# Kernel tuning notes

Hardware: AMD Instinct MI355X
Metric: run time of the kernel (lower is better)

Reference implementation:

```python
import jax, jax.numpy as jnp
import numpy as np

INPUT_SIZE = 1024
HIDDEN = 1024
NUM_LAYERS = 1
BATCH = 64
SEQ = 512


def setup_inputs() -> dict:
    key = jax.random.key(0)
    ks = jax.random.split(key, 5)
    stdv = 1.0 / np.sqrt(HIDDEN)
    u = lambda k, shape: jax.random.uniform(k, shape, jnp.float32, -stdv, stdv)
    x = jax.random.normal(ks[0], (BATCH, SEQ, INPUT_SIZE), dtype=jnp.float32)
    Wi = u(ks[1], (INPUT_SIZE, 4 * HIDDEN))
    Wh = u(ks[2], (HIDDEN, 4 * HIDDEN))
    bi = u(ks[3], (4 * HIDDEN,))
    bh = u(ks[4], (4 * HIDDEN,))
    return {"x": x, "Wi": Wi, "Wh": Wh, "bi": bi, "bh": bh}


def reference(x, Wi, Wh, bi, bh):
    B, T, _ = x.shape
    H = Wh.shape[0]
    L = NUM_LAYERS
    h0 = jnp.zeros((L, B, H), x.dtype)
    c0 = jnp.zeros((L, B, H), x.dtype)
    b = bi + bh  # fuse bias add

    def step(carry, xt):
        h, c = carry
        gates = xt @ Wi + h[-1] @ Wh + b  # [B, 4H]
        i_g, f_g, g_g, o_g = jnp.split(gates, 4, axis=1)
        i_g = jax.nn.sigmoid(i_g)
        f_g = jax.nn.sigmoid(f_g)
        g_g = jnp.tanh(g_g)
        o_g = jax.nn.sigmoid(o_g)
        c = f_g * c + i_g * g_g          # broadcasts [B,H] over [L,B,H]
        h = o_g * jnp.tanh(c)
        return (h, c), h

    (h, c), hs = jax.lax.scan(step, (h0, c0), jnp.swapaxes(x, 0, 1))
    # hs: [T, L, B, H] -> output [L, T, B, H] matching torch cat along dim=1
    output = jnp.swapaxes(hs, 0, 1)
    return output, h, c
```

## Files before the change

### kernel.cpp

```cpp
#include <hip/hip_runtime.h>
#include <math.h>

#define I_SZ 1024
#define H_SZ 1024
#define FH   4096
#define B_SZ 64
#define T_SZ 512

typedef _Float16 half8 __attribute__((ext_vector_type(8)));
typedef float    f32x4 __attribute__((ext_vector_type(4)));

#define MiB (1u << 20)
#define SLOT_HALFS 65536


__global__ __launch_bounds__(256) void k_cvt_wT(const float* __restrict__ W,
                                                _Float16* __restrict__ WT) {
  int tid = blockIdx.x * 256 + threadIdx.x;
  int n  = tid & (FH - 1);
  int k8 = tid >> 12;
  half8 h;
#pragma unroll
  for (int j = 0; j < 8; j++) h[j] = (_Float16)W[(size_t)(k8 * 8 + j) * FH + n];
  *(half8*)(WT + (size_t)n * 1024 + k8 * 8) = h;
}

__global__ __launch_bounds__(256) void k_gemm_pre(
    const float* __restrict__ x, const _Float16* __restrict__ WiT,
    const float* __restrict__ bi, const float* __restrict__ bh,
    _Float16* __restrict__ G) {
  __shared__ _Float16 As[128][40];
  __shared__ _Float16 Bs[128][40];
  const int tn = blockIdx.x, tm = blockIdx.y;
  const int tx = threadIdx.x;
  const int l = tx & 63, wv = tx >> 6;
  const int wm = wv & 1, wn = wv >> 1;
  const int r0 = tx >> 2, q0 = tx & 3;
  const int m0 = tm * 128 + r0, m1 = m0 + 64;
  const float* aR0 = x + (size_t)((m0 & 63) * T_SZ + (m0 >> 6)) * I_SZ + q0 * 8;
  const float* aR1 = x + (size_t)((m1 & 63) * T_SZ + (m1 >> 6)) * I_SZ + q0 * 8;
  const _Float16* bR0 = WiT + (size_t)(tn * 128 + r0) * 1024 + q0 * 8;
  const _Float16* bR1 = WiT + (size_t)(tn * 128 + 64 + r0) * 1024 + q0 * 8;

  f32x4 acc[4][4];
#pragma unroll
  for (int a = 0; a < 4; a++)
#pragma unroll
    for (int b = 0; b < 4; b++) acc[a][b] = {0.f, 0.f, 0.f, 0.f};

  for (int kt = 0; kt < 32; kt++) {
    __syncthreads();
    float4 va0 = *(const float4*)(aR0 + kt * 32);
    float4 va1 = *(const float4*)(aR0 + kt * 32 + 4);
    float4 vb0 = *(const float4*)(aR1 + kt * 32);
    float4 vb1 = *(const float4*)(aR1 + kt * 32 + 4);
    half8 ha, hb;
    ha[0] = (_Float16)va0.x; ha[1] = (_Float16)va0.y; ha[2] = (_Float16)va0.z; ha[3] = (_Float16)va0.w;
    ha[4] = (_Float16)va1.x; ha[5] = (_Float16)va1.y; ha[6] = (_Float16)va1.z; ha[7] = (_Float16)va1.w;
    hb[0] = (_Float16)vb0.x; hb[1] = (_Float16)vb0.y; hb[2] = (_Float16)vb0.z; hb[3] = (_Float16)vb0.w;
    hb[4] = (_Float16)vb1.x; hb[5] = (_Float16)vb1.y; hb[6] = (_Float16)vb1.z; hb[7] = (_Float16)vb1.w;
    *(half8*)(&As[r0][q0 * 8])      = ha;
    *(half8*)(&As[64 + r0][q0 * 8]) = hb;
    *(half8*)(&Bs[r0][q0 * 8])      = *(const half8*)(bR0 + kt * 32);
    *(half8*)(&Bs[64 + r0][q0 * 8]) = *(const half8*)(bR1 + kt * 32);
    __syncthreads();
    half8 af[4], bf[4];
#pragma unroll
    for (int i = 0; i < 4; i++) {
      af[i] = *(const half8*)(&As[wm * 64 + i * 16 + (l & 15)][(l >> 4) * 8]);
      bf[i] = *(const half8*)(&Bs[wn * 64 + i * 16 + (l & 15)][(l >> 4) * 8]);
    }
#pragma unroll
    for (int i = 0; i < 4; i++)
#pragma unroll
      for (int j2 = 0; j2 < 4; j2++)
        acc[i][j2] = __builtin_amdgcn_mfma_f32_16x16x32_f16(af[i], bf[j2], acc[i][j2], 0, 0, 0);
  }
#pragma unroll
  for (int j2 = 0; j2 < 4; j2++) {
    const int col = tn * 128 + wn * 64 + j2 * 16 + (l & 15);
    const float bias = bi[col] + bh[col];
#pragma unroll
    for (int i = 0; i < 4; i++) {
      const int mb = tm * 128 + wm * 64 + i * 16 + ((l >> 4) << 2);
#pragma unroll
      for (int r = 0; r < 4; r++)
        G[(size_t)(mb + r) * FH + col] = (_Float16)(acc[i][j2][r] + bias);
    }
  }
}

__global__ __launch_bounds__(256, 1) void k_lstm(
    const _Float16* __restrict__ WhT, const _Float16* __restrict__ G,
    _Float16* __restrict__ hdb, float* __restrict__ out, int* ctrl) {
  __shared__ float gt[4][16][17];
  const int wg = blockIdx.x;
  const int jbase = wg * 4;
  const int tx = threadIdx.x;
  const int l = tx & 63, wv = tx >> 6;
  const int cc = l & 15;
  const int cg = cc >> 2, cj = cc & 3;
  const int kb = (l >> 4) * 8;
  const int am = 16 * wv + cc;
  const int mrow0 = 16 * wv + ((l >> 4) << 2);
  const int gcol = cg * 1024 + jbase + cj;
  const int lrow = l & 15;
  const int brow = 16 * wv + lrow;

  int* flags = ctrl + 256;
  const half8* bp = (const half8*)(WhT + (size_t)gcol * 1024 + kb);

  float cst[4] = {0.f, 0.f, 0.f, 0.f};
  float hl[4]  = {0.f, 0.f, 0.f, 0.f};

  for (int t = 0; t < T_SZ; t++) {
    const _Float16* hb = hdb + (size_t)(t & 1) * SLOT_HALFS;
    _Float16* hn = hdb + (size_t)((t & 1) ^ 1) * SLOT_HALFS;

    _Float16 gp[4];
    const _Float16* Gt = G + (size_t)(t * 64 + mrow0) * FH + gcol;
#pragma unroll
    for (int r = 0; r < 4; r++) gp[r] = Gt[(size_t)r * FH];

    f32x4 acc = {0.f, 0.f, 0.f, 0.f};
    const unsigned long long* ap = (const unsigned long long*)(hb + am * 1024 + kb);
    unsigned long long a0[16], a1[16];
    half8 bf[16];
#pragma unroll
    for (int p = 0; p < 16; p++) {
      a0[p] = __hip_atomic_load(ap + p * 8, __ATOMIC_RELAXED, __HIP_MEMORY_SCOPE_SYSTEM);
      a1[p] = __hip_atomic_load(ap + p * 8 + 1, __ATOMIC_RELAXED, __HIP_MEMORY_SCOPE_SYSTEM);
      bf[p] = bp[p * 4];
    }
#pragma unroll
    for (int ki = 0; ki < 32; ki++) {
      union { unsigned long long u[2]; half8 h; } cv;
      cv.u[0] = a0[ki & 15]; cv.u[1] = a1[ki & 15];
      half8 b = bf[ki & 15];
      if (ki < 16) {
        a0[ki & 15] = __hip_atomic_load(ap + (ki + 16) * 8, __ATOMIC_RELAXED, __HIP_MEMORY_SCOPE_SYSTEM);
        a1[ki & 15] = __hip_atomic_load(ap + (ki + 16) * 8 + 1, __ATOMIC_RELAXED, __HIP_MEMORY_SCOPE_SYSTEM);
        bf[ki & 15] = bp[(ki + 16) * 4];
      }
      acc = __builtin_amdgcn_mfma_f32_16x16x32_f16(cv.h, b, acc, 0, 0, 0);
    }

#pragma unroll
    for (int r = 0; r < 4; r++)
      gt[wv][((l >> 4) << 2) + r][cc] = acc[r] + (float)gp[r];

    if (l < 16) {
      float hv[4];
#pragma unroll
      for (int j = 0; j < 4; j++) {
        float gi = gt[wv][lrow][0 + j];
        float gf = gt[wv][lrow][4 + j];
        float gg = gt[wv][lrow][8 + j];
        float go = gt[wv][lrow][12 + j];
        float ig = 1.f / (1.f + expf(-gi));
        float fg = 1.f / (1.f + expf(-gf));
        float gv = tanhf(gg);
        float og = 1.f / (1.f + expf(-go));
        cst[j] = fg * cst[j] + ig * gv;
        hv[j] = og * tanhf(cst[j]);
        hl[j] = hv[j];
      }
      *(float4*)(out + (size_t)t * (B_SZ * H_SZ) + brow * H_SZ + jbase) =
          make_float4(hv[0], hv[1], hv[2], hv[3]);
      union { _Float16 h[4]; unsigned long long u; } pk;
#pragma unroll
      for (int j = 0; j < 4; j++) pk.h[j] = (_Float16)hv[j];
      __hip_atomic_store((unsigned long long*)(hn + brow * H_SZ + jbase), pk.u,
                         __ATOMIC_RELAXED, __HIP_MEMORY_SCOPE_SYSTEM);
    }

    if (t + 1 < T_SZ) {
      asm volatile("s_waitcnt vmcnt(0)" ::: "memory");
      __syncthreads();
      if (tx == 0)
        __hip_atomic_store(flags + wg, t + 1, __ATOMIC_RELAXED,
                           __HIP_MEMORY_SCOPE_SYSTEM);
      if (wv == 0) {
        const int target = t + 1;
        const unsigned long long* fp = (const unsigned long long*)flags;
        int guard = 0;
        for (;;) {
          unsigned long long f0 = __hip_atomic_load(fp + l, __ATOMIC_RELAXED,
                                                    __HIP_MEMORY_SCOPE_SYSTEM);
          unsigned long long f1 = __hip_atomic_load(fp + 64 + l, __ATOMIC_RELAXED,
                                                    __HIP_MEMORY_SCOPE_SYSTEM);
          bool ok = ((int)(f0 & 0xffffffffu) >= target) &&
                    ((int)(f0 >> 32) >= target) &&
                    ((int)(f1 & 0xffffffffu) >= target) &&
                    ((int)(f1 >> 32) >= target);
          if (__all(ok)) break;
          if (++guard > (1 << 24)) break;
          __builtin_amdgcn_s_sleep(1);
        }
      }
      __syncthreads();
    }
  }

  if (l < 16) {
    const size_t ob = (size_t)T_SZ * (B_SZ * H_SZ);
    *(float4*)(out + ob + brow * H_SZ + jbase) = make_float4(hl[0], hl[1], hl[2], hl[3]);
    *(float4*)(out + ob + B_SZ * H_SZ + brow * H_SZ + jbase) =
        make_float4(cst[0], cst[1], cst[2], cst[3]);
  }
}

extern "C" void kernel_launch(void* const* d_in, const int* in_sizes, int n_in,
                              void* d_out, int out_size, void* d_ws, size_t ws_size,
                              hipStream_t stream) {
  (void)in_sizes; (void)n_in; (void)out_size; (void)ws_size;
  const float* x  = (const float*)d_in[0];
  const float* Wi = (const float*)d_in[1];
  const float* Wh = (const float*)d_in[2];
  const float* bi = (const float*)d_in[3];
  const float* bh = (const float*)d_in[4];
  float* out = (float*)d_out;
  char* ws = (char*)d_ws;

  int* ctrl     = (int*)ws;
  _Float16* hdb = (_Float16*)(ws + 4096);
  _Float16* WhT = (_Float16*)(ws + (size_t)1 * MiB);
  _Float16* WiT = (_Float16*)(ws + (size_t)16 * MiB);
  _Float16* G   = (_Float16*)(ws + (size_t)32 * MiB);

  hipMemsetAsync(ws, 0, 4096 + 2 * SLOT_HALFS * sizeof(_Float16), stream);
  k_cvt_wT<<<2048, 256, 0, stream>>>(Wi, WiT);
  k_cvt_wT<<<2048, 256, 0, stream>>>(Wh, WhT);
  dim3 g2(32, 256);
  k_gemm_pre<<<g2, 256, 0, stream>>>(x, WiT, bi, bh, G);
  k_lstm<<<256, 256, 0, stream>>>(WhT, G, hdb, out, ctrl);
}
```

Baseline: 8.198 ms.

## Halve persistent LSTM workgroups and stage h in swizzled LDS

Restructures the persistent recurrent kernel from 256 workgroups of 256 threads to 128 workgroups of 512 threads, each owning 8 hidden units. Each step the whole fp16 h vector is copied cooperatively into XOR-swizzled shared memory and the MFMA A operands are read from LDS instead of per-wave global atomic loads. Step 0 skips the recurrent matmul, and the flag barrier polls half as many flags with a longer sleep. The aim is lower grid-barrier latency and less redundant global h traffic per step, at the cost of a full 128KB LDS copy every step and fewer CUs doing the matmul.

New measurement: 8.838 ms. +7.8%, slower.

```diff
diff --git a/kernel.cpp b/kernel.cpp
--- a/kernel.cpp
+++ b/kernel.cpp
@@ -6,6 +6,8 @@
 #define FH   4096
 #define B_SZ 64
 #define T_SZ 512
+#define NWG  128
+#define NTHR 512
 
 typedef _Float16 half8 __attribute__((ext_vector_type(8)));
 typedef float    f32x4 __attribute__((ext_vector_type(4)));
@@ -90,22 +92,25 @@
   }
 }
 
-__global__ __launch_bounds__(256, 1) void k_lstm(
+__global__ __launch_bounds__(NTHR, 1) void k_lstm(
     const _Float16* __restrict__ WhT, const _Float16* __restrict__ G,
     _Float16* __restrict__ hdb, float* __restrict__ out, int* ctrl) {
-  __shared__ float gt[4][16][17];
+  __shared__ _Float16 hstage[B_SZ * H_SZ];
+  __shared__ float gates[B_SZ][36];
+
   const int wg = blockIdx.x;
-  const int jbase = wg * 4;
+  const int jb = wg * 8;
   const int tx = threadIdx.x;
   const int l = tx & 63, wv = tx >> 6;
+  const int wm = wv & 3;
+  const int wn = wv >> 2;
   const int cc = l & 15;
-  const int cg = cc >> 2, cj = cc & 3;
+  const int crow = 16 * wm + cc;
+  const int cB = 16 * wn + cc;
+  const int gcol = (cB >> 3) * 1024 + jb + (cB & 7);
   const int kb = (l >> 4) * 8;
-  const int am = 16 * wv + cc;
-  const int mrow0 = 16 * wv + ((l >> 4) << 2);
-  const int gcol = cg * 1024 + jbase + cj;
-  const int lrow = l & 15;
-  const int brow = 16 * wv + lrow;
+  const int cb = tx >> 1;
+  const int cq = (tx & 1) * 4;
 
   int* flags = ctrl + 256;
   const half8* bp = (const half8*)(WhT + (size_t)gcol * 1024 + kb);
@@ -114,64 +119,88 @@
   float hl[4]  = {0.f, 0.f, 0.f, 0.f};
 
   for (int t = 0; t < T_SZ; t++) {
-    const _Float16* hb = hdb + (size_t)(t & 1) * SLOT_HALFS;
-    _Float16* hn = hdb + (size_t)((t & 1) ^ 1) * SLOT_HALFS;
-
-    _Float16 gp[4];
-    const _Float16* Gt = G + (size_t)(t * 64 + mrow0) * FH + gcol;
-#pragma unroll
-    for (int r = 0; r < 4; r++) gp[r] = Gt[(size_t)r * FH];
-
-    f32x4 acc = {0.f, 0.f, 0.f, 0.f};
-    const unsigned long long* ap = (const unsigned long long*)(hb + am * 1024 + kb);
-    unsigned long long a0[16], a1[16];
-    half8 bf[16];
-#pragma unroll
-    for (int p = 0; p < 16; p++) {
-      a0[p] = __hip_atomic_load(ap + p * 8, __ATOMIC_RELAXED, __HIP_MEMORY_SCOPE_SYSTEM);
-      a1[p] = __hip_atomic_load(ap + p * 8 + 1, __ATOMIC_RELAXED, __HIP_MEMORY_SCOPE_SYSTEM);
-      bf[p] = bp[p * 4];
-    }
-#pragma unroll
-    for (int ki = 0; ki < 32; ki++) {
-      union { unsigned long long u[2]; half8 h; } cv;
-      cv.u[0] = a0[ki & 15]; cv.u[1] = a1[ki & 15];
-      half8 b = bf[ki & 15];
-      if (ki < 16) {
-        a0[ki & 15] = __hip_atomic_load(ap + (ki + 16) * 8, __ATOMIC_RELAXED, __HIP_MEMORY_SCOPE_SYSTEM);
-        a1[ki & 15] = __hip_atomic_load(ap + (ki + 16) * 8 + 1, __ATOMIC_RELAXED, __HIP_MEMORY_SCOPE_SYSTEM);
-        bf[ki & 15] = bp[(ki + 16) * 4];
-      }
-      acc = __builtin_amdgcn_mfma_f32_16x16x32_f16(cv.h, b, acc, 0, 0, 0);
-    }
-
-#pragma unroll
-    for (int r = 0; r < 4; r++)
-      gt[wv][((l >> 4) << 2) + r][cc] = acc[r] + (float)gp[r];
-
-    if (l < 16) {
+    unsigned long long gv[4] = {0, 0, 0, 0};
+    if (tx < 128) {
+#pragma unroll
+      for (int g4 = 0; g4 < 4; g4++)
+        gv[g4] = *(const unsigned long long*)(
+            G + (size_t)(t * 64 + cb) * FH + g4 * 1024 + jb + cq);
+    }
+
+    if (t > 0) {
+      const _Float16* hb = hdb + (size_t)(t & 1) * SLOT_HALFS;
+      const unsigned long long* hb64 = (const unsigned long long*)hb;
+      unsigned long long u0[16], u1[16];
+#pragma unroll
+      for (int i = 0; i < 16; i++) {
+        const int c = i * NTHR + tx;
+        u0[i] = __hip_atomic_load(hb64 + (size_t)c * 2,
+                                  __ATOMIC_RELAXED, __HIP_MEMORY_SCOPE_SYSTEM);
+        u1[i] = __hip_atomic_load(hb64 + (size_t)c * 2 + 1,
+                                  __ATOMIC_RELAXED, __HIP_MEMORY_SCOPE_SYSTEM);
+      }
+#pragma unroll
+      for (int i = 0; i < 16; i++) {
+        const int c = i * NTHR + tx;
+        const int r_ = c >> 7;
+        const int b_ = r_ * 2048 + (((c & 127) << 4) ^ ((r_ & 7) << 4));
+        union { unsigned long long u[2]; f32x4 v; } w;
+        w.u[0] = u0[i]; w.u[1] = u1[i];
+        *(f32x4*)((char*)hstage + b_) = w.v;
+      }
+    }
+    __syncthreads();
+
+    if (t > 0) {
+      f32x4 acc = {0.f, 0.f, 0.f, 0.f};
+      const char* hsb = (const char*)hstage;
+      const int rbase = crow * 2048;
+      const int sw = (crow & 7) << 4;
+      half8 bf[16];
+#pragma unroll
+      for (int p = 0; p < 16; p++) bf[p] = bp[p * 4];
+#pragma unroll
+      for (int ki = 0; ki < 32; ki++) {
+        half8 b = bf[ki & 15];
+        half8 af = *(const half8*)(hsb + rbase + ((ki * 64 + ((l >> 4) << 4)) ^ sw));
+        if (ki < 16) bf[ki & 15] = bp[(ki + 16) * 4];
+        acc = __builtin_amdgcn_mfma_f32_16x16x32_f16(af, b, acc, 0, 0, 0);
+      }
+#pragma unroll
+      for (int r = 0; r < 4; r++)
+        gates[16 * wm + ((l >> 4) << 2) + r][cB] = acc[r];
+    } else {
+      for (int i = tx; i < B_SZ * 36; i += NTHR) ((float*)gates)[i] = 0.f;
+    }
+    __syncthreads();
+
+    if (tx < 128) {
       float hv[4];
 #pragma unroll
       for (int j = 0; j < 4; j++) {
-        float gi = gt[wv][lrow][0 + j];
-        float gf = gt[wv][lrow][4 + j];
-        float gg = gt[wv][lrow][8 + j];
-        float go = gt[wv][lrow][12 + j];
+        const int jj = cq + j;
+        union { unsigned long long u; _Float16 h[4]; } u0g, u1g, u2g, u3g;
+        u0g.u = gv[0]; u1g.u = gv[1]; u2g.u = gv[2]; u3g.u = gv[3];
+        float gi = gates[cb][ 0 + jj] + (float)u0g.h[j];
+        float gf = gates[cb][ 8 + jj] + (float)u1g.h[j];
+        float gg = gates[cb][16 + jj] + (float)u2g.h[j];
+        float go = gates[cb][24 + jj] + (float)u3g.h[j];
         float ig = 1.f / (1.f + expf(-gi));
         float fg = 1.f / (1.f + expf(-gf));
-        float gv = tanhf(gg);
+        float gvv = tanhf(gg);
         float og = 1.f / (1.f + expf(-go));
-        cst[j] = fg * cst[j] + ig * gv;
+        cst[j] = fg * cst[j] + ig * gvv;
         hv[j] = og * tanhf(cst[j]);
         hl[j] = hv[j];
       }
-      *(float4*)(out + (size_t)t * (B_SZ * H_SZ) + brow * H_SZ + jbase) =
+      *(float4*)(out + (size_t)t * (B_SZ * H_SZ) + (size_t)cb * H_SZ + jb + cq) =
           make_float4(hv[0], hv[1], hv[2], hv[3]);
       union { _Float16 h[4]; unsigned long long u; } pk;
 #pragma unroll
       for (int j = 0; j < 4; j++) pk.h[j] = (_Float16)hv[j];
-      __hip_atomic_store((unsigned long long*)(hn + brow * H_SZ + jbase), pk.u,
-                         __ATOMIC_RELAXED, __HIP_MEMORY_SCOPE_SYSTEM);
+      _Float16* hn = hdb + (size_t)((t & 1) ^ 1) * SLOT_HALFS;
+      __hip_atomic_store((unsigned long long*)(hn + (size_t)cb * H_SZ + jb + cq),
+                         pk.u, __ATOMIC_RELAXED, __HIP_MEMORY_SCOPE_SYSTEM);
     }
 
     if (t + 1 < T_SZ) {
@@ -187,25 +216,22 @@
         for (;;) {
           unsigned long long f0 = __hip_atomic_load(fp + l, __ATOMIC_RELAXED,
                                                     __HIP_MEMORY_SCOPE_SYSTEM);
-          unsigned long long f1 = __hip_atomic_load(fp + 64 + l, __ATOMIC_RELAXED,
-                                                    __HIP_MEMORY_SCOPE_SYSTEM);
           bool ok = ((int)(f0 & 0xffffffffu) >= target) &&
-                    ((int)(f0 >> 32) >= target) &&
-                    ((int)(f1 & 0xffffffffu) >= target) &&
-                    ((int)(f1 >> 32) >= target);
+                    ((int)(f0 >> 32) >= target);
           if (__all(ok)) break;
-          if (++guard > (1 << 24)) break;
-          __builtin_amdgcn_s_sleep(1);
+          if (++guard > (1 << 20)) break;
+          __builtin_amdgcn_s_sleep(4);
         }
       }
       __syncthreads();
     }
   }
 
-  if (l < 16) {
+  if (tx < 128) {
     const size_t ob = (size_t)T_SZ * (B_SZ * H_SZ);
-    *(float4*)(out + ob + brow * H_SZ + jbase) = make_float4(hl[0], hl[1], hl[2], hl[3]);
-    *(float4*)(out + ob + B_SZ * H_SZ + brow * H_SZ + jbase) =
+    *(float4*)(out + ob + (size_t)cb * H_SZ + jb + cq) =
+        make_float4(hl[0], hl[1], hl[2], hl[3]);
+    *(float4*)(out + ob + B_SZ * H_SZ + (size_t)cb * H_SZ + jb + cq) =
         make_float4(cst[0], cst[1], cst[2], cst[3]);
   }
 }
@@ -228,10 +254,10 @@
   _Float16* WiT = (_Float16*)(ws + (size_t)16 * MiB);
   _Float16* G   = (_Float16*)(ws + (size_t)32 * MiB);
 
-  hipMemsetAsync(ws, 0, 4096 + 2 * SLOT_HALFS * sizeof(_Float16), stream);
+  (void)hipMemsetAsync(ws, 0, 4096, stream);
   k_cvt_wT<<<2048, 256, 0, stream>>>(Wi, WiT);
   k_cvt_wT<<<2048, 256, 0, stream>>>(Wh, WhT);
   dim3 g2(32, 256);
   k_gemm_pre<<<g2, 256, 0, stream>>>(x, WiT, bi, bh, G);
-  k_lstm<<<256, 256, 0, stream>>>(WhT, G, hdb, out, ctrl);
-}
+  k_lstm<<<NWG, NTHR, 0, stream>>>(WhT, G, hdb, out, ctrl);
+}
```
